# Performance work log

Measured on AMD Instinct MI355X. Metric: run time of the kernel, lower is better.

## Reference

```python
import jax, jax.numpy as jnp
import numpy as np

N_USERS = 100000
N_ITEMS = 100000
EMBED_DIM = 64
N_LAYERS = 3
NNZ = 1000000


def setup_inputs() -> dict:
    key = jax.random.key(0)
    k1, k2, k3, k4, k5 = jax.random.split(key, 5)
    N = N_USERS + N_ITEMS
    user_w = jax.random.normal(k1, (N_USERS, EMBED_DIM), dtype=jnp.float32) * 0.1
    item_w = jax.random.normal(k2, (N_ITEMS, EMBED_DIM), dtype=jnp.float32) * 0.1
    vals = jax.random.uniform(k3, (NNZ,), dtype=jnp.float32)
    rows = jax.random.randint(k4, (NNZ,), 0, N, dtype=jnp.int64 if jax.config.jax_enable_x64 else jnp.int32)
    cols = jax.random.randint(k5, (NNZ,), 0, N, dtype=jnp.int64 if jax.config.jax_enable_x64 else jnp.int32)
    return {"user_w": user_w, "item_w": item_w, "vals": vals, "rows": rows, "cols": cols}


def _spmm(vals, rows, cols, x, n):
    # sparse [n,n] COO  @  dense [n,d]  ->  [n,d]
    gathered = vals[:, None] * x[cols]          # [nnz, d]
    return jax.ops.segment_sum(gathered, rows, num_segments=n)


def reference(user_w, item_w, vals, rows, cols):
    # LightGCN-style propagation (SimGCL.propagate, perturb=False)
    n = user_w.shape[0] + item_w.shape[0]
    x = jnp.concatenate([user_w, item_w], axis=0)   # [N, d]
    acc = x                                         # running sum over layer stack
    for _ in range(N_LAYERS):
        x = _spmm(vals, rows, cols, x, n)
        acc = acc + x
    out = acc / jnp.asarray(N_LAYERS + 1, dtype=acc.dtype)  # mean over stacked embs
    return out[: user_w.shape[0]], out[user_w.shape[0]:]
```

## Files before the change

kernel.cpp:

```cpp
#include <hip/hip_runtime.h>
#include <hip/hip_bf16.h>
#include <hip/hip_fp16.h>

#define EMB 64
#define BSHIFT 11
#define BROWS (1 << BSHIFT)
#define NBMAX 128
#define TILE 4096

__device__ __forceinline__ float ld_elem(const void* p, long long i, int bf) {
    if (bf) return (float)((const __hip_bfloat16*)p)[i];
    return ((const float*)p)[i];
}

__device__ __forceinline__ float4 ld4_x0(const void* uw, const void* iw,
                                         int n_user_elems, long long e, int bf) {
    const void* base = uw;
    if (e >= (long long)n_user_elems) { base = iw; e -= n_user_elems; }
    if (bf) {
        uint2 r = *reinterpret_cast<const uint2*>((const unsigned short*)base + e);
        return make_float4(__uint_as_float((r.x & 0xFFFFu) << 16),
                           __uint_as_float(r.x & 0xFFFF0000u),
                           __uint_as_float((r.y & 0xFFFFu) << 16),
                           __uint_as_float(r.y & 0xFFFF0000u));
    }
    return *reinterpret_cast<const float4*>((const float*)base + e);
}

__device__ __forceinline__ float4 ld4_f16(const __half* g, long long e) {
    uint2 r = *reinterpret_cast<const uint2*>(g + e);
    union { unsigned int u; __half2 h; } c0, c1;
    c0.u = r.x; c1.u = r.y;
    float2 f0 = __half22float2(c0.h), f1 = __half22float2(c1.h);
    return make_float4(f0.x, f0.y, f1.x, f1.y);
}

__global__ void hist_coarse(const int* __restrict__ rows, int* __restrict__ counts, int nnz,
                            const unsigned short* __restrict__ v16, int* __restrict__ flag) {
    __shared__ int h[NBMAX];
    int t = threadIdx.x;
    if (t < NBMAX) h[t] = 0;
    __syncthreads();
    int tid = blockIdx.x * blockDim.x + t;
    int stride = gridDim.x * blockDim.x;
    for (int e = tid; e < nnz; e += stride) atomicAdd(&h[rows[e] >> BSHIFT], 1);
    __syncthreads();
    if (t < NBMAX) { int v = h[t]; if (v) atomicAdd(&counts[t], v); }
    if (tid == 0) {
        int hits = 0;
        for (int i = 0; i < 256; ++i) {
            unsigned int hb = v16[i] >> 8;
            unsigned int ex = hb & 0x7F;
            if (hb < 0x80 && ex >= 0x30 && ex < 0x40) hits++;
        }
        *flag = (hits >= 200) ? 1 : 0;
    }
}

__global__ void scan_coarse(const int* __restrict__ counts, int* __restrict__ cptr,
                            int* __restrict__ bcur, int nb) {
    __shared__ int lds[128];
    int t = threadIdx.x;
    int v = (t < nb) ? counts[t] : 0;
    lds[t] = v;
    __syncthreads();
    for (int off = 1; off < 128; off <<= 1) {
        int x = lds[t];
        int a = (t >= off) ? lds[t - off] : 0;
        __syncthreads();
        lds[t] = x + a;
        __syncthreads();
    }
    if (t < nb) { int excl = lds[t] - v; cptr[t] = excl; bcur[t] = excl; }
    if (t == 0) cptr[nb] = lds[127];
}

__global__ void bucket_scatter(const void* __restrict__ vals, const int* __restrict__ rows,
                               const int* __restrict__ cols, int* __restrict__ bcur,
                               float2* __restrict__ staged, int nnz, int nbuck,
                               const int* __restrict__ flagp) {
    __shared__ int hist[NBMAX];
    __shared__ int exb[NBMAX];
    __shared__ int gb[NBMAX];
    __shared__ int sc[NBMAX];
    __shared__ float2 st[TILE];
    __shared__ int bkt[TILE];
    int t = threadIdx.x;
    int bf = *flagp;

    for (int tile = blockIdx.x * TILE; tile < nnz; tile += gridDim.x * TILE) {
        int cnt = min(TILE, nnz - tile);
        for (int i = t; i < NBMAX; i += 256) hist[i] = 0;
        __syncthreads();

        int   myb[16], myo[16], mmeta[16];
        float mv[16];
#pragma unroll
        for (int k = 0; k < 16; ++k) {
            int i = tile + k * 256 + t;
            if (i < nnz && (k * 256 + t) < cnt) {
                int r = rows[i], c = cols[i];
                mv[k]    = ld_elem(vals, i, bf);
                myb[k]   = r >> BSHIFT;
                mmeta[k] = ((r & (BROWS - 1)) << 18) | c;
                myo[k]   = atomicAdd(&hist[myb[k]], 1);
            } else myb[k] = -1;
        }
        __syncthreads();

        if (t < NBMAX) sc[t] = hist[t];
        __syncthreads();
        for (int off = 1; off < NBMAX; off <<= 1) {
            int v = 0;
            if (t < NBMAX) { v = sc[t]; if (t >= off) v += sc[t - off]; }
            __syncthreads();
            if (t < NBMAX) sc[t] = v;
            __syncthreads();
        }
        if (t < NBMAX) {
            exb[t] = sc[t] - hist[t];
            if (t < nbuck && hist[t] > 0) gb[t] = atomicAdd(&bcur[t], hist[t]);
        }
        __syncthreads();

#pragma unroll
        for (int k = 0; k < 16; ++k) {
            if (myb[k] >= 0) {
                int p = exb[myb[k]] + myo[k];
                st[p]  = make_float2(mv[k], __int_as_float(mmeta[k]));
                bkt[p] = myb[k];
            }
        }
        __syncthreads();

        for (int p = t; p < cnt; p += 256) {
            int b = bkt[p];
            staged[gb[b] + (p - exb[b])] = st[p];
        }
        __syncthreads();
    }
}

__global__ void bucket_csr(const int* __restrict__ cptr,
                           const float2* __restrict__ staged,
                           float2* __restrict__ edges,
                           int* __restrict__ row_ptr, int nrows, int nbuck) {
    __shared__ int rcnt[BROWS];
    __shared__ int ssum[256];
    int b = blockIdx.x;
    int t = threadIdx.x;
    int cbeg = cptr[b], cend = cptr[b + 1];
    int rlo = b << BSHIFT;
    int nr = min(BROWS, nrows - rlo);

    for (int i = t; i < BROWS; i += 256) rcnt[i] = 0;
    __syncthreads();

    const int* sm = (const int*)staged;
    for (int i = cbeg + t; i < cend; i += 256) {
        int lr = (sm[2 * i + 1] >> 18) & (BROWS - 1);
        atomicAdd(&rcnt[lr], 1);
    }
    __syncthreads();

    int base = t * 8;
    int loc[8]; int s = 0;
#pragma unroll
    for (int k = 0; k < 8; ++k) { loc[k] = rcnt[base + k]; s += loc[k]; }
    ssum[t] = s;
    __syncthreads();
    for (int off = 1; off < 256; off <<= 1) {
        int x = ssum[t];
        int a = (t >= off) ? ssum[t - off] : 0;
        __syncthreads();
        ssum[t] = x + a;
        __syncthreads();
    }
    int run = (t > 0) ? ssum[t - 1] : 0;
#pragma unroll
    for (int k = 0; k < 8; ++k) { int c = loc[k]; rcnt[base + k] = run; run += c; }
    __syncthreads();

    for (int i = t; i < nr; i += 256) row_ptr[rlo + i] = cbeg + rcnt[i];
    if (b == nbuck - 1 && t == 0) row_ptr[nrows] = cend;

    for (int i = cbeg + t; i < cend; i += 256) {
        float2 rec = staged[i];
        int meta = __float_as_int(rec.y);
        int lr = (meta >> 18) & (BROWS - 1);
        int c  = meta & 0x3FFFF;
        int pos = atomicAdd(&rcnt[lr], 1);
        edges[cbeg + pos] = make_float2(rec.x, __int_as_float(c));
    }
}

template <int GMODE, int OMODE>
__global__ void spmm_csr4(const int* __restrict__ row_ptr,
                          const float2* __restrict__ edges,
                          const void* __restrict__ uw, const void* __restrict__ iw,
                          int n_user_elems,
                          const __half* __restrict__ gin, void* __restrict__ gout,
                          int nrows, const int* __restrict__ flagp) {
    int tid  = blockIdx.x * blockDim.x + threadIdx.x;
    int wave = tid >> 6;
    int lane = threadIdx.x & 63;
    int g    = lane >> 4;
    int l    = lane & 15;
    int wid  = wave * 4 + g;
    if (wid >= nrows) return;
    int bf = *flagp;
    int beg = row_ptr[wid], end = row_ptr[wid + 1];
    float a0 = 0.f, a1 = 0.f, a2 = 0.f, a3 = 0.f;

#define GATHER(E, X) { \
        long long ce = (long long)__float_as_int((E).y) * EMB + l * 4; \
        if (GMODE == 0) X = ld4_x0(uw, iw, n_user_elems, ce, bf); \
        else            X = ld4_f16(gin, ce); }
#define ACC(E, X) { a0 += (E).x * (X).x; a1 += (E).x * (X).y; \
                    a2 += (E).x * (X).z; a3 += (E).x * (X).w; }

    int j = beg;
    for (; j + 4 <= end; j += 4) {
        float2 e0 = edges[j], e1 = edges[j + 1], e2 = edges[j + 2], e3 = edges[j + 3];
        float4 xa, xb, xc, xd;
        GATHER(e0, xa); GATHER(e1, xb); GATHER(e2, xc); GATHER(e3, xd);
        ACC(e0, xa); ACC(e1, xb); ACC(e2, xc); ACC(e3, xd);
    }
    if (j + 2 <= end) {
        float2 e0 = edges[j], e1 = edges[j + 1];
        float4 xa, xb;
        GATHER(e0, xa); GATHER(e1, xb);
        ACC(e0, xa); ACC(e1, xb);
        j += 2;
    }
    if (j < end) {
        float2 e0 = edges[j];
        float4 xa; GATHER(e0, xa);
        ACC(e0, xa);
    }
#undef GATHER
#undef ACC

    long long re = (long long)wid * EMB + l * 4;
    float4 x0v = ld4_x0(uw, iw, n_user_elems, re, bf);
    float o0 = x0v.x + a0, o1 = x0v.y + a1, o2 = x0v.z + a2, o3 = x0v.w + a3;

    if (OMODE == 1) {
        __half2 h01 = __floats2half2_rn(o0, o1);
        __half2 h23 = __floats2half2_rn(o2, o3);
        union { __half2 h; unsigned int u; } p0, p1;
        p0.h = h01; p1.h = h23;
        uint2 out; out.x = p0.u; out.y = p1.u;
        reinterpret_cast<uint2*>(gout)[re >> 2] = out;
    } else {
        o0 *= 0.25f; o1 *= 0.25f; o2 *= 0.25f; o3 *= 0.25f;
        if (bf) {
            __hip_bfloat16 b0 = (__hip_bfloat16)o0, b1 = (__hip_bfloat16)o1;
            __hip_bfloat16 b2 = (__hip_bfloat16)o2, b3 = (__hip_bfloat16)o3;
            unsigned short s0 = *reinterpret_cast<unsigned short*>(&b0);
            unsigned short s1 = *reinterpret_cast<unsigned short*>(&b1);
            unsigned short s2 = *reinterpret_cast<unsigned short*>(&b2);
            unsigned short s3 = *reinterpret_cast<unsigned short*>(&b3);
            uint2 out;
            out.x = (unsigned int)s0 | ((unsigned int)s1 << 16);
            out.y = (unsigned int)s2 | ((unsigned int)s3 << 16);
            reinterpret_cast<uint2*>(gout)[re >> 2] = out;
        } else {
            reinterpret_cast<float4*>(gout)[re >> 2] = make_float4(o0, o1, o2, o3);
        }
    }
}

extern "C" void kernel_launch(void* const* d_in, const int* in_sizes, int n_in,
                              void* d_out, int out_size, void* d_ws, size_t ws_size,
                              hipStream_t stream) {
    const void* uw   = d_in[0];
    const void* iw   = d_in[1];
    const void* vals = d_in[2];
    const int*  rows = (const int*)d_in[3];
    const int*  cols = (const int*)d_in[4];

    const int n_user = in_sizes[0];
    const int total  = in_sizes[0] + in_sizes[1];
    const int nnz    = in_sizes[2];
    const int nrows  = total / EMB;
    const int nbuck  = (nrows + BROWS - 1) >> BSHIFT;

    char* p = (char*)d_ws;
    auto alloc = [&](size_t bytes) { char* q = p; p += (bytes + 255) & ~(size_t)255; return q; };
    int*    flag    = (int*)   alloc(sizeof(int));
    int*    counts  = (int*)   alloc(NBMAX * sizeof(int));
    int*    cptr    = (int*)   alloc((NBMAX + 1) * sizeof(int));
    int*    bcur    = (int*)   alloc(NBMAX * sizeof(int));
    int*    row_ptr = (int*)   alloc((size_t)(nrows + 1) * sizeof(int));
    float2* staged  = (float2*)alloc((size_t)nnz * sizeof(float2));
    float2* edges   = (float2*)alloc((size_t)nnz * sizeof(float2));
    size_t used = (size_t)(p - (char*)d_ws);
    size_t avail = (ws_size > used) ? ws_size - used : 0;

    const size_t g_f16 = (size_t)total * sizeof(__half);
    __half *g2, *g3;
    if (avail >= 2 * g_f16 + 512) { g2 = (__half*)alloc(g_f16); g3 = (__half*)alloc(g_f16); }
    else { g2 = (__half*)d_out; g3 = (__half*)alloc(g_f16); }

    hipMemsetAsync(counts, 0, NBMAX * sizeof(int), stream);
    hist_coarse<<<120, 256, 0, stream>>>(rows, counts, nnz, (const unsigned short*)vals, flag);
    scan_coarse<<<1, 128, 0, stream>>>(counts, cptr, bcur, nbuck);
    const int ntiles = (nnz + TILE - 1) / TILE;
    bucket_scatter<<<ntiles, 256, 0, stream>>>(vals, rows, cols, bcur, staged, nnz, nbuck, flag);
    bucket_csr<<<nbuck, 256, 0, stream>>>(cptr, staged, edges, row_ptr, nrows, nbuck);

    const int nwaves = (nrows + 3) / 4;
    const int rb = (nwaves * 64 + 255) / 256;
    spmm_csr4<0, 1><<<rb, 256, 0, stream>>>(row_ptr, edges, uw, iw, n_user,
                                            nullptr, g2, nrows, flag);
    spmm_csr4<1, 1><<<rb, 256, 0, stream>>>(row_ptr, edges, uw, iw, n_user,
                                            g2, g3, nrows, flag);
    spmm_csr4<1, 3><<<rb, 256, 0, stream>>>(row_ptr, edges, uw, iw, n_user,
                                            g3, d_out, nrows, flag);
}
```

Measured before the change: 272.1 us.

## Process each SpMM row with 8 lanes using 16-byte gathers; widen CSR build blocks

The SpMM kernels now assign 8 lanes per row instead of 16, and each lane loads 8 elements (a 16-byte vector) per gathered neighbour, so a wave covers 8 rows. The aim is fewer, wider memory transactions per gather and more rows in flight per wave. The bucket_csr kernel moves to 512 threads per block, and the dtype probe in hist_coarse is spread across block 0's threads instead of running as a serial loop. The trade-off is more registers per lane and potentially more load imbalance within a wave, because 8 rows of varying degree now share it.

```diff
diff --git a/kernel.cpp b/kernel.cpp
--- a/kernel.cpp
+++ b/kernel.cpp
@@ -13,48 +13,62 @@
     return ((const float*)p)[i];
 }
 
-__device__ __forceinline__ float4 ld4_x0(const void* uw, const void* iw,
-                                         int n_user_elems, long long e, int bf) {
+struct f8 { float4 a, b; };
+
+__device__ __forceinline__ f8 ld8_x0(const void* uw, const void* iw,
+                                     int n_user_elems, long long e, int bf) {
     const void* base = uw;
     if (e >= (long long)n_user_elems) { base = iw; e -= n_user_elems; }
+    f8 r;
     if (bf) {
-        uint2 r = *reinterpret_cast<const uint2*>((const unsigned short*)base + e);
-        return make_float4(__uint_as_float((r.x & 0xFFFFu) << 16),
-                           __uint_as_float(r.x & 0xFFFF0000u),
-                           __uint_as_float((r.y & 0xFFFFu) << 16),
-                           __uint_as_float(r.y & 0xFFFF0000u));
-    }
-    return *reinterpret_cast<const float4*>((const float*)base + e);
-}
-
-__device__ __forceinline__ float4 ld4_f16(const __half* g, long long e) {
-    uint2 r = *reinterpret_cast<const uint2*>(g + e);
-    union { unsigned int u; __half2 h; } c0, c1;
-    c0.u = r.x; c1.u = r.y;
-    float2 f0 = __half22float2(c0.h), f1 = __half22float2(c1.h);
-    return make_float4(f0.x, f0.y, f1.x, f1.y);
+        uint4 q = *reinterpret_cast<const uint4*>((const unsigned short*)base + e);
+        r.a = make_float4(__uint_as_float((q.x & 0xFFFFu) << 16),
+                          __uint_as_float(q.x & 0xFFFF0000u),
+                          __uint_as_float((q.y & 0xFFFFu) << 16),
+                          __uint_as_float(q.y & 0xFFFF0000u));
+        r.b = make_float4(__uint_as_float((q.z & 0xFFFFu) << 16),
+                          __uint_as_float(q.z & 0xFFFF0000u),
+                          __uint_as_float((q.w & 0xFFFFu) << 16),
+                          __uint_as_float(q.w & 0xFFFF0000u));
+    } else {
+        const float4* f = reinterpret_cast<const float4*>((const float*)base + e);
+        r.a = f[0]; r.b = f[1];
+    }
+    return r;
+}
+
+__device__ __forceinline__ f8 ld8_f16(const __half* g, long long e) {
+    uint4 q = *reinterpret_cast<const uint4*>(g + e);
+    union { unsigned int u; __half2 h; } c;
+    f8 r;
+    c.u = q.x; float2 f0 = __half22float2(c.h);
+    c.u = q.y; float2 f1 = __half22float2(c.h);
+    c.u = q.z; float2 f2 = __half22float2(c.h);
+    c.u = q.w; float2 f3 = __half22float2(c.h);
+    r.a = make_float4(f0.x, f0.y, f1.x, f1.y);
+    r.b = make_float4(f2.x, f2.y, f3.x, f3.y);
+    return r;
 }
 
 __global__ void hist_coarse(const int* __restrict__ rows, int* __restrict__ counts, int nnz,
                             const unsigned short* __restrict__ v16, int* __restrict__ flag) {
     __shared__ int h[NBMAX];
+    __shared__ int probe;
     int t = threadIdx.x;
     if (t < NBMAX) h[t] = 0;
+    if (t == 0) probe = 0;
     __syncthreads();
     int tid = blockIdx.x * blockDim.x + t;
     int stride = gridDim.x * blockDim.x;
     for (int e = tid; e < nnz; e += stride) atomicAdd(&h[rows[e] >> BSHIFT], 1);
+    if (blockIdx.x == 0) {
+        unsigned int hb = v16[t] >> 8;
+        unsigned int ex = hb & 0x7F;
+        if (hb < 0x80 && ex >= 0x30 && ex < 0x40) atomicAdd(&probe, 1);
+    }
     __syncthreads();
     if (t < NBMAX) { int v = h[t]; if (v) atomicAdd(&counts[t], v); }
-    if (tid == 0) {
-        int hits = 0;
-        for (int i = 0; i < 256; ++i) {
-            unsigned int hb = v16[i] >> 8;
-            unsigned int ex = hb & 0x7F;
-            if (hb < 0x80 && ex >= 0x30 && ex < 0x40) hits++;
-        }
-        *flag = (hits >= 200) ? 1 : 0;
-    }
+    if (blockIdx.x == 0 && t == 0) *flag = (probe >= 200) ? 1 : 0;
 }
 
 __global__ void scan_coarse(const int* __restrict__ counts, int* __restrict__ cptr,
@@ -146,30 +160,30 @@
                            float2* __restrict__ edges,
                            int* __restrict__ row_ptr, int nrows, int nbuck) {
     __shared__ int rcnt[BROWS];
-    __shared__ int ssum[256];
+    __shared__ int ssum[512];
     int b = blockIdx.x;
     int t = threadIdx.x;
     int cbeg = cptr[b], cend = cptr[b + 1];
     int rlo = b << BSHIFT;
     int nr = min(BROWS, nrows - rlo);
 
-    for (int i = t; i < BROWS; i += 256) rcnt[i] = 0;
+    for (int i = t; i < BROWS; i += 512) rcnt[i] = 0;
     __syncthreads();
 
     const int* sm = (const int*)staged;
-    for (int i = cbeg + t; i < cend; i += 256) {
+    for (int i = cbeg + t; i < cend; i += 512) {
         int lr = (sm[2 * i + 1] >> 18) & (BROWS - 1);
         atomicAdd(&rcnt[lr], 1);
     }
     __syncthreads();
 
-    int base = t * 8;
-    int loc[8]; int s = 0;
+    int base = t * 4;
+    int loc[4]; int s = 0;
 #pragma unroll
-    for (int k = 0; k < 8; ++k) { loc[k] = rcnt[base + k]; s += loc[k]; }
+    for (int k = 0; k < 4; ++k) { loc[k] = rcnt[base + k]; s += loc[k]; }
     ssum[t] = s;
     __syncthreads();
-    for (int off = 1; off < 256; off <<= 1) {
+    for (int off = 1; off < 512; off <<= 1) {
         int x = ssum[t];
         int a = (t >= off) ? ssum[t - off] : 0;
         __syncthreads();
@@ -178,13 +192,13 @@
     }
     int run = (t > 0) ? ssum[t - 1] : 0;
 #pragma unroll
-    for (int k = 0; k < 8; ++k) { int c = loc[k]; rcnt[base + k] = run; run += c; }
-    __syncthreads();
-
-    for (int i = t; i < nr; i += 256) row_ptr[rlo + i] = cbeg + rcnt[i];
+    for (int k = 0; k < 4; ++k) { int c = loc[k]; rcnt[base + k] = run; run += c; }
+    __syncthreads();
+
+    for (int i = t; i < nr; i += 512) row_ptr[rlo + i] = cbeg + rcnt[i];
     if (b == nbuck - 1 && t == 0) row_ptr[nrows] = cend;
 
-    for (int i = cbeg + t; i < cend; i += 256) {
+    for (int i = cbeg + t; i < cend; i += 512) {
         float2 rec = staged[i];
         int meta = __float_as_int(rec.y);
         int lr = (meta >> 18) & (BROWS - 1);
@@ -195,7 +209,7 @@
 }
 
 template <int GMODE, int OMODE>
-__global__ void spmm_csr4(const int* __restrict__ row_ptr,
+__global__ void spmm_csr8(const int* __restrict__ row_ptr,
                           const float2* __restrict__ edges,
                           const void* __restrict__ uw, const void* __restrict__ iw,
                           int n_user_elems,
@@ -204,69 +218,88 @@
     int tid  = blockIdx.x * blockDim.x + threadIdx.x;
     int wave = tid >> 6;
     int lane = threadIdx.x & 63;
-    int g    = lane >> 4;
-    int l    = lane & 15;
-    int wid  = wave * 4 + g;
+    int g    = lane >> 3;
+    int l    = lane & 7;
+    int wid  = wave * 8 + g;
     if (wid >= nrows) return;
     int bf = *flagp;
     int beg = row_ptr[wid], end = row_ptr[wid + 1];
-    float a0 = 0.f, a1 = 0.f, a2 = 0.f, a3 = 0.f;
+    float4 accA = make_float4(0.f, 0.f, 0.f, 0.f);
+    float4 accB = make_float4(0.f, 0.f, 0.f, 0.f);
 
 #define GATHER(E, X) { \
-        long long ce = (long long)__float_as_int((E).y) * EMB + l * 4; \
-        if (GMODE == 0) X = ld4_x0(uw, iw, n_user_elems, ce, bf); \
-        else            X = ld4_f16(gin, ce); }
-#define ACC(E, X) { a0 += (E).x * (X).x; a1 += (E).x * (X).y; \
-                    a2 += (E).x * (X).z; a3 += (E).x * (X).w; }
+        long long ce = (long long)__float_as_int((E).y) * EMB + l * 8; \
+        if (GMODE == 0) X = ld8_x0(uw, iw, n_user_elems, ce, bf); \
+        else            X = ld8_f16(gin, ce); }
+#define ACC(E, X) { float v = (E).x; \
+        accA.x += v * (X).a.x; accA.y += v * (X).a.y; \
+        accA.z += v * (X).a.z; accA.w += v * (X).a.w; \
+        accB.x += v * (X).b.x; accB.y += v * (X).b.y; \
+        accB.z += v * (X).b.z; accB.w += v * (X).b.w; }
 
     int j = beg;
     for (; j + 4 <= end; j += 4) {
         float2 e0 = edges[j], e1 = edges[j + 1], e2 = edges[j + 2], e3 = edges[j + 3];
-        float4 xa, xb, xc, xd;
+        f8 xa, xb, xc, xd;
         GATHER(e0, xa); GATHER(e1, xb); GATHER(e2, xc); GATHER(e3, xd);
         ACC(e0, xa); ACC(e1, xb); ACC(e2, xc); ACC(e3, xd);
     }
     if (j + 2 <= end) {
         float2 e0 = edges[j], e1 = edges[j + 1];
-        float4 xa, xb;
+        f8 xa, xb;
         GATHER(e0, xa); GATHER(e1, xb);
         ACC(e0, xa); ACC(e1, xb);
         j += 2;
     }
     if (j < end) {
         float2 e0 = edges[j];
-        float4 xa; GATHER(e0, xa);
+        f8 xa; GATHER(e0, xa);
         ACC(e0, xa);
     }
 #undef GATHER
 #undef ACC
 
-    long long re = (long long)wid * EMB + l * 4;
-    float4 x0v = ld4_x0(uw, iw, n_user_elems, re, bf);
-    float o0 = x0v.x + a0, o1 = x0v.y + a1, o2 = x0v.z + a2, o3 = x0v.w + a3;
+    long long re = (long long)wid * EMB + l * 8;
+    f8 x0v = ld8_x0(uw, iw, n_user_elems, re, bf);
+    float o0 = x0v.a.x + accA.x, o1 = x0v.a.y + accA.y;
+    float o2 = x0v.a.z + accA.z, o3 = x0v.a.w + accA.w;
+    float o4 = x0v.b.x + accB.x, o5 = x0v.b.y + accB.y;
+    float o6 = x0v.b.z + accB.z, o7 = x0v.b.w + accB.w;
 
     if (OMODE == 1) {
-        __half2 h01 = __floats2half2_rn(o0, o1);
-        __half2 h23 = __floats2half2_rn(o2, o3);
-        union { __half2 h; unsigned int u; } p0, p1;
-        p0.h = h01; p1.h = h23;
-        uint2 out; out.x = p0.u; out.y = p1.u;
-        reinterpret_cast<uint2*>(gout)[re >> 2] = out;
+        union { __half2 h; unsigned int u; } p0, p1, p2, p3;
+        p0.h = __floats2half2_rn(o0, o1);
+        p1.h = __floats2half2_rn(o2, o3);
+        p2.h = __floats2half2_rn(o4, o5);
+        p3.h = __floats2half2_rn(o6, o7);
+        uint4 out; out.x = p0.u; out.y = p1.u; out.z = p2.u; out.w = p3.u;
+        *reinterpret_cast<uint4*>((__half*)gout + re) = out;
     } else {
         o0 *= 0.25f; o1 *= 0.25f; o2 *= 0.25f; o3 *= 0.25f;
+        o4 *= 0.25f; o5 *= 0.25f; o6 *= 0.25f; o7 *= 0.25f;
         if (bf) {
             __hip_bfloat16 b0 = (__hip_bfloat16)o0, b1 = (__hip_bfloat16)o1;
             __hip_bfloat16 b2 = (__hip_bfloat16)o2, b3 = (__hip_bfloat16)o3;
+            __hip_bfloat16 b4 = (__hip_bfloat16)o4, b5 = (__hip_bfloat16)o5;
+            __hip_bfloat16 b6 = (__hip_bfloat16)o6, b7 = (__hip_bfloat16)o7;
             unsigned short s0 = *reinterpret_cast<unsigned short*>(&b0);
             unsigned short s1 = *reinterpret_cast<unsigned short*>(&b1);
             unsigned short s2 = *reinterpret_cast<unsigned short*>(&b2);
             unsigned short s3 = *reinterpret_cast<unsigned short*>(&b3);
-            uint2 out;
+            unsigned short s4 = *reinterpret_cast<unsigned short*>(&b4);
+            unsigned short s5 = *reinterpret_cast<unsigned short*>(&b5);
+            unsigned short s6 = *reinterpret_cast<unsigned short*>(&b6);
+            unsigned short s7 = *reinterpret_cast<unsigned short*>(&b7);
+            uint4 out;
             out.x = (unsigned int)s0 | ((unsigned int)s1 << 16);
             out.y = (unsigned int)s2 | ((unsigned int)s3 << 16);
-            reinterpret_cast<uint2*>(gout)[re >> 2] = out;
+            out.z = (unsigned int)s4 | ((unsigned int)s5 << 16);
+            out.w = (unsigned int)s6 | ((unsigned int)s7 << 16);
+            *reinterpret_cast<uint4*>((unsigned short*)gout + re) = out;
         } else {
-            reinterpret_cast<float4*>(gout)[re >> 2] = make_float4(o0, o1, o2, o3);
+            float4* fp = reinterpret_cast<float4*>((float*)gout + re);
+            fp[0] = make_float4(o0, o1, o2, o3);
+            fp[1] = make_float4(o4, o5, o6, o7);
         }
     }
 }
@@ -308,14 +341,14 @@
     scan_coarse<<<1, 128, 0, stream>>>(counts, cptr, bcur, nbuck);
     const int ntiles = (nnz + TILE - 1) / TILE;
     bucket_scatter<<<ntiles, 256, 0, stream>>>(vals, rows, cols, bcur, staged, nnz, nbuck, flag);
-    bucket_csr<<<nbuck, 256, 0, stream>>>(cptr, staged, edges, row_ptr, nrows, nbuck);
-
-    const int nwaves = (nrows + 3) / 4;
+    bucket_csr<<<nbuck, 512, 0, stream>>>(cptr, staged, edges, row_ptr, nrows, nbuck);
+
+    const int nwaves = (nrows + 7) / 8;
     const int rb = (nwaves * 64 + 255) / 256;
-    spmm_csr4<0, 1><<<rb, 256, 0, stream>>>(row_ptr, edges, uw, iw, n_user,
+    spmm_csr8<0, 1><<<rb, 256, 0, stream>>>(row_ptr, edges, uw, iw, n_user,
                                             nullptr, g2, nrows, flag);
-    spmm_csr4<1, 1><<<rb, 256, 0, stream>>>(row_ptr, edges, uw, iw, n_user,
+    spmm_csr8<1, 1><<<rb, 256, 0, stream>>>(row_ptr, edges, uw, iw, n_user,
                                             g2, g3, nrows, flag);
-    spmm_csr4<1, 3><<<rb, 256, 0, stream>>>(row_ptr, edges, uw, iw, n_user,
+    spmm_csr8<1, 3><<<rb, 256, 0, stream>>>(row_ptr, edges, uw, iw, n_user,
                                             g3, d_out, nrows, flag);
 }
```

Result: faster. 254.7 us (-6.4%).
